# Kernel optimization log

Measured on AMD Instinct MI355X. Metric: run time of the kernel, lower is better.

Reference implementation:

```python
import jax, jax.numpy as jnp
import numpy as np

B, N, M, F = 32, 1024, 1024, 64


def setup_inputs() -> dict:
    key = jax.random.key(0)
    kx, ky = jax.random.split(key)
    x = jax.random.normal(kx, (B, N, F), dtype=jnp.float32)
    y = jax.random.normal(ky, (B, M, F), dtype=jnp.float32)
    return {"x": x, "y": y}


def _cdist(x, y):
    # torch.cdist(x, y, p=2): [N, M] euclidean distance matrix via GEMM form
    sq = (jnp.sum(x * x, axis=-1)[:, None]
          + jnp.sum(y * y, axis=-1)[None, :]
          - 2.0 * (x @ y.T))
    return jnp.sqrt(jnp.maximum(sq, 0.0))


def _dtw_single(x, y):
    # Classic DTW DP: D[i,j] = cost[i,j] + min(D[i-1,j], D[i,j-1], D[i-1,j-1])
    # with D[0,0]=0 and inf boundaries. The inner (j) recurrence
    #   cur[j] = cost[j] + min(m[j], cur[j-1]),  m[j] = min(prev[j], prev[j-1])
    # is a min-plus prefix scan solvable in closed form:
    #   cur[j] = C[j] + cummin_j(cost[j] + m[j] - C[j]),  C = cumsum(cost)
    # which vectorizes each row (wavefront-equivalent, no O(M) python loop).
    dist = _cdist(x, y)  # [N, M]
    m = dist.shape[1]
    init = jnp.concatenate([jnp.zeros((1,), dist.dtype),
                            jnp.full((m,), jnp.inf, dist.dtype)])  # D[0, :]

    def row_step(prev, cost_row):
        mins = jnp.minimum(prev[1:], prev[:-1])          # min(up, diag), [M]
        C = jnp.cumsum(cost_row)                         # [M]
        cur = C + jax.lax.cummin(cost_row + mins - C)    # [M]
        prev_new = jnp.concatenate(
            [jnp.full((1,), jnp.inf, dist.dtype), cur])  # D[i, 0] = inf
        return prev_new, None

    last, _ = jax.lax.scan(row_step, init, dist)
    return last[-1]  # D[N, M]


def reference(x, y):
    # batched forward, distances per pair: [B]
    return jax.vmap(_dtw_single)(x, y)
```

## Files before the change

### kernel.cpp

```cpp
#include <hip/hip_runtime.h>
#include <math.h>

#define BB 32
#define NN 1024
#define MM 1024
#define FF 64
#define INF_ 1e30f

typedef float f32x4 __attribute__((ext_vector_type(4)));

__global__ __launch_bounds__(256) void cost_kernel(const float* __restrict__ x,
                                                   const float* __restrict__ y,
                                                   float* __restrict__ cost) {
    __shared__ float Xs[FF][68];
    __shared__ float Ys[FF][68];
    __shared__ float xnl[64];
    __shared__ float ynl[64];
    const int b    = blockIdx.z;
    const int row0 = blockIdx.y * 64;
    const int col0 = blockIdx.x * 64;
    const int tid  = threadIdx.x;
    const float* xb = x + (size_t)b * NN * FF;
    const float* yb = y + (size_t)b * MM * FF;

    #pragma unroll
    for (int cc = 0; cc < 4; ++cc) {
        int s  = tid + cc * 256;
        int r  = s >> 4;
        int kq = s & 15;
        float4 vx = *(const float4*)(xb + (size_t)(row0 + r) * FF + kq * 4);
        float4 vy = *(const float4*)(yb + (size_t)(col0 + r) * FF + kq * 4);
        Xs[kq*4+0][r] = vx.x; Xs[kq*4+1][r] = vx.y; Xs[kq*4+2][r] = vx.z; Xs[kq*4+3][r] = vx.w;
        Ys[kq*4+0][r] = vy.x; Ys[kq*4+1][r] = vy.y; Ys[kq*4+2][r] = vy.z; Ys[kq*4+3][r] = vy.w;
    }
    __syncthreads();

    if (tid < 64) {
        float s = 0.0f;
        #pragma unroll 16
        for (int k = 0; k < FF; ++k) { float v = Xs[k][tid]; s += v * v; }
        xnl[tid] = s;
    } else if (tid < 128) {
        int r = tid - 64;
        float s = 0.0f;
        #pragma unroll 16
        for (int k = 0; k < FF; ++k) { float v = Ys[k][r]; s += v * v; }
        ynl[r] = s;
    }

    const int tx = tid & 15, ty = tid >> 4;
    float acc[4][4] = {};
    #pragma unroll 16
    for (int k = 0; k < FF; ++k) {
        float4 a  = *(const float4*)&Xs[k][ty * 4];
        float4 bb = *(const float4*)&Ys[k][tx * 4];
        float av[4] = {a.x, a.y, a.z, a.w};
        float bv[4] = {bb.x, bb.y, bb.z, bb.w};
        #pragma unroll
        for (int r = 0; r < 4; ++r)
            #pragma unroll
            for (int c = 0; c < 4; ++c)
                acc[r][c] += av[r] * bv[c];
    }
    __syncthreads();

    float* cD = cost + (size_t)b * NN * MM;
    #pragma unroll
    for (int r = 0; r < 4; ++r) {
        int rl  = ty * 4 + r;
        int row = row0 + rl;
        float xnv = xnl[rl];
        #pragma unroll
        for (int c = 0; c < 4; ++c) {
            int cl  = tx * 4 + c;
            int col = col0 + cl;
            float v = xnv + ynl[cl] - 2.0f * acc[r][c];
            v = sqrtf(fmaxf(v, 0.0f));
            cD[(size_t)((row + col) & 1023) * MM + row] = v;
        }
    }
}

__device__ __forceinline__ float dpp_wave_shr1(float v, float oldv) {
    int t = __builtin_amdgcn_update_dpp(__float_as_int(oldv), __float_as_int(v),
                                        0x138, 0xf, 0xf, false);
    return __int_as_float(t);
}

struct RowBuf { f32x4 q0, q1, q2, q3; };

__device__ __forceinline__ void issue_row(RowBuf& R, const float* rowbase,
                                          unsigned voff) {
    asm volatile(
        "global_load_dwordx4 %0, %4, %5\n\t"
        "global_load_dwordx4 %1, %4, %5 offset:16\n\t"
        "global_load_dwordx4 %2, %4, %5 offset:32\n\t"
        "global_load_dwordx4 %3, %4, %5 offset:48"
        : "=v"(R.q0), "=v"(R.q1), "=v"(R.q2), "=v"(R.q3)
        : "v"(voff), "s"(rowbase));
}

__device__ __forceinline__ void touch_row(float& dummy, const float* rowbase,
                                          unsigned voff) {
    asm volatile("global_load_dword %0, %1, %2"
                 : "+v"(dummy) : "v"(voff), "s"(rowbase));
}

__global__ __launch_bounds__(64)
__attribute__((amdgpu_waves_per_eu(1, 1)))
void dtw_diag_kernel(const float* __restrict__ cost, float* __restrict__ out) {
    const int b    = blockIdx.x;
    const int lane = threadIdx.x;
    const float* cbD = cost + (size_t)b * NN * MM;
    const unsigned voff = (unsigned)lane * 64u;

    RowBuf R0, R1, R2, R3, R4, R5, R6, R7;
    float dummy = 0.0f;
    issue_row(R0, cbD + 0 * (size_t)MM, voff);  touch_row(dummy, cbD +  8 * (size_t)MM, voff);
    issue_row(R1, cbD + 1 * (size_t)MM, voff);  touch_row(dummy, cbD +  9 * (size_t)MM, voff);
    issue_row(R2, cbD + 2 * (size_t)MM, voff);  touch_row(dummy, cbD + 10 * (size_t)MM, voff);
    issue_row(R3, cbD + 3 * (size_t)MM, voff);  touch_row(dummy, cbD + 11 * (size_t)MM, voff);
    issue_row(R4, cbD + 4 * (size_t)MM, voff);  touch_row(dummy, cbD + 12 * (size_t)MM, voff);
    issue_row(R5, cbD + 5 * (size_t)MM, voff);  touch_row(dummy, cbD + 13 * (size_t)MM, voff);
    issue_row(R6, cbD + 6 * (size_t)MM, voff);  touch_row(dummy, cbD + 14 * (size_t)MM, voff);
    issue_row(R7, cbD + 7 * (size_t)MM, voff);  touch_row(dummy, cbD + 15 * (size_t)MM, voff);

    float A[16], B[16];
    #pragma unroll
    for (int j = 0; j < 16; ++j) { A[j] = INF_; B[j] = INF_; }
    float bnd = 0.0f;

    #define DIAG_STEP(Rk, PV, P2, NR, NT)                                      \
    {                                                                          \
        float pvm1 = dpp_wave_shr1(PV[15], INF_);                              \
        float p2m1 = dpp_wave_shr1(P2[15], bnd);                               \
        float t[16];                                                           \
        _Pragma("unroll")                                                      \
        for (int r = 0; r < 16; ++r) {                                         \
            float pv_r = PV[r], p2_r = P2[r];                                  \
            t[r] = fminf(fminf(pv_r, pvm1), p2m1);                             \
            pvm1 = pv_r; p2m1 = p2_r;                                          \
        }                                                                      \
        asm volatile("s_waitcnt vmcnt(36)" ::: "memory");                      \
        __builtin_amdgcn_sched_barrier(0);                                     \
        float cc[16] = {Rk.q0[0], Rk.q0[1], Rk.q0[2], Rk.q0[3],                \
                        Rk.q1[0], Rk.q1[1], Rk.q1[2], Rk.q1[3],                \
                        Rk.q2[0], Rk.q2[1], Rk.q2[2], Rk.q2[3],                \
                        Rk.q3[0], Rk.q3[1], Rk.q3[2], Rk.q3[3]};               \
        _Pragma("unroll")                                                      \
        for (int r = 0; r < 16; ++r) P2[r] = cc[r] + t[r];                     \
        __builtin_amdgcn_sched_barrier(0);                                     \
        issue_row(Rk, cbD + (size_t)(NR) * MM, voff);                          \
        touch_row(dummy, cbD + (size_t)(NT) * MM, voff);                       \
    }

    DIAG_STEP(R0, A, B, 8,  16)   bnd = INF_;
    DIAG_STEP(R1, B, A, 9,  17)
    DIAG_STEP(R2, A, B, 10, 18)
    DIAG_STEP(R3, B, A, 11, 19)
    DIAG_STEP(R4, A, B, 12, 20)
    DIAG_STEP(R5, B, A, 13, 21)
    DIAG_STEP(R6, A, B, 14, 22)
    DIAG_STEP(R7, B, A, 15, 23)

    for (int d0 = 8; d0 < 2040; d0 += 8) {
        DIAG_STEP(R0, A, B, ((d0 +  8) & 1023), ((d0 + 16) & 1023))
        DIAG_STEP(R1, B, A, ((d0 +  9) & 1023), ((d0 + 17) & 1023))
        DIAG_STEP(R2, A, B, ((d0 + 10) & 1023), ((d0 + 18) & 1023))
        DIAG_STEP(R3, B, A, ((d0 + 11) & 1023), ((d0 + 19) & 1023))
        DIAG_STEP(R4, A, B, ((d0 + 12) & 1023), ((d0 + 20) & 1023))
        DIAG_STEP(R5, B, A, ((d0 + 13) & 1023), ((d0 + 21) & 1023))
        DIAG_STEP(R6, A, B, ((d0 + 14) & 1023), ((d0 + 22) & 1023))
        DIAG_STEP(R7, B, A, ((d0 + 15) & 1023), ((d0 + 23) & 1023))
    }

    DIAG_STEP(R0, A, B, 0, 16)
    DIAG_STEP(R1, B, A, 1, 17)
    DIAG_STEP(R2, A, B, 2, 18)
    DIAG_STEP(R3, B, A, 3, 19)
    DIAG_STEP(R4, A, B, 4, 20)
    DIAG_STEP(R5, B, A, 5, 21)
    DIAG_STEP(R6, A, B, 6, 22)
    #undef DIAG_STEP

    asm volatile("" :: "v"(dummy));

    if (lane == 63) out[b] = B[15];
}

__global__ __launch_bounds__(1024) void dtw_fused_kernel(const float* __restrict__ x,
                                                         const float* __restrict__ y,
                                                         float* __restrict__ out) {
    const int b    = blockIdx.x;
    const int tid  = threadIdx.x;
    const int lane = tid & 63;
    const int wid  = tid >> 6;
    __shared__ float P[MM];
    __shared__ float xrow[FF];
    __shared__ float part_sum[16];
    __shared__ float part_min[16];

    float yr[FF];
    const float* yrow = y + ((size_t)b * MM + tid) * FF;
    #pragma unroll
    for (int q = 0; q < FF / 4; ++q) {
        float4 v = ((const float4*)yrow)[q];
        yr[q*4+0] = v.x; yr[q*4+1] = v.y; yr[q*4+2] = v.z; yr[q*4+3] = v.w;
    }

    P[tid] = INF_;
    __syncthreads();

    const float* xb = x + (size_t)b * NN * FF;
    float result = 0.0f;

    for (int i = 0; i < NN; ++i) {
        if (tid < FF) xrow[tid] = xb[(size_t)i * FF + tid];
        float up   = P[tid];
        float diag = (tid == 0) ? (i == 0 ? 0.0f : INF_) : P[tid - 1];
        float m    = fminf(up, diag);
        __syncthreads();

        float ss = 0.0f;
        #pragma unroll 16
        for (int k = 0; k < FF; ++k) {
            float d = xrow[k] - yr[k];
            ss += d * d;
        }
        float c = sqrtf(ss);

        float s = c;
        #pragma unroll
        for (int d = 1; d < 64; d <<= 1) {
            float t = __shfl_up(s, d, 64);
            if (lane >= d) s += t;
        }
        if (lane == 63) part_sum[wid] = s;
        __syncthreads();
        if (tid < 16) {
            float p = part_sum[tid];
            #pragma unroll
            for (int d = 1; d < 16; d <<= 1) {
                float t = __shfl_up(p, d, 64);
                if (tid >= d) p += t;
            }
            part_sum[tid] = p;
        }
        __syncthreads();
        float C = s + (wid > 0 ? part_sum[wid - 1] : 0.0f);

        float z = c + m - C;
        float w = z;
        #pragma unroll
        for (int d = 1; d < 64; d <<= 1) {
            float t = __shfl_up(w, d, 64);
            if (lane >= d) w = fminf(w, t);
        }
        if (lane == 63) part_min[wid] = w;
        __syncthreads();
        if (tid < 16) {
            float p = part_min[tid];
            #pragma unroll
            for (int d = 1; d < 16; d <<= 1) {
                float t = __shfl_up(p, d, 64);
                if (tid >= d) p = fminf(p, t);
            }
            part_min[tid] = p;
        }
        __syncthreads();
        float wm  = (wid > 0) ? fminf(w, part_min[wid - 1]) : w;
        float cur = C + wm;

        P[tid] = cur;
        __syncthreads();
        if (i == NN - 1 && tid == MM - 1) result = cur;
    }
    if (tid == MM - 1) out[b] = result;
}

extern "C" void kernel_launch(void* const* d_in, const int* in_sizes, int n_in,
                              void* d_out, int out_size, void* d_ws, size_t ws_size,
                              hipStream_t stream) {
    const float* x = (const float*)d_in[0];
    const float* y = (const float*)d_in[1];
    float* out = (float*)d_out;

    size_t need = (size_t)BB * NN * MM * sizeof(float);

    if (ws_size >= need) {
        float* cost = (float*)d_ws;
        hipLaunchKernelGGL(cost_kernel, dim3(MM / 64, NN / 64, BB), dim3(256), 0, stream,
                           x, y, cost);
        hipLaunchKernelGGL(dtw_diag_kernel, dim3(BB), dim3(64), 0, stream, cost, out);
    } else {
        hipLaunchKernelGGL(dtw_fused_kernel, dim3(BB), dim3(1024), 0, stream, x, y, out);
    }
}
```

Measured before the change: 291.5 us.

## Store DTW cost matrix as bf16 and deepen diagonal prefetch pipeline

The cost kernel now writes the skewed cost matrix in bf16 (round-to-nearest-even), halving workspace traffic for both the write and the DTW scan's reads. The diagonal kernel loads half-size rows, unpacks them to fp32 in registers, and keeps 16 rows in flight instead of 8 plus touch prefetches, with the wait count adjusted to match. Accumulating 2047 bf16-rounded costs adds error to the final DTW distance, which may exceed tolerance.

```diff
diff --git a/kernel.cpp b/kernel.cpp
--- a/kernel.cpp
+++ b/kernel.cpp
@@ -11,7 +11,7 @@
 
 __global__ __launch_bounds__(256) void cost_kernel(const float* __restrict__ x,
                                                    const float* __restrict__ y,
-                                                   float* __restrict__ cost) {
+                                                   unsigned short* __restrict__ cost) {
     __shared__ float Xs[FF][68];
     __shared__ float Ys[FF][68];
     __shared__ float xnl[64];
@@ -64,7 +64,7 @@
     }
     __syncthreads();
 
-    float* cD = cost + (size_t)b * NN * MM;
+    unsigned short* cB = cost + (size_t)b * NN * MM;
     #pragma unroll
     for (int r = 0; r < 4; ++r) {
         int rl  = ty * 4 + r;
@@ -76,7 +76,9 @@
             int col = col0 + cl;
             float v = xnv + ynl[cl] - 2.0f * acc[r][c];
             v = sqrtf(fmaxf(v, 0.0f));
-            cD[(size_t)((row + col) & 1023) * MM + row] = v;
+            unsigned bb_ = __float_as_uint(v);
+            bb_ += 0x7FFFu + ((bb_ >> 16) & 1u);
+            cB[(size_t)((row + col) & 1023) * MM + row] = (unsigned short)(bb_ >> 16);
         }
     }
 }
@@ -87,50 +89,61 @@
     return __int_as_float(t);
 }
 
-struct RowBuf { f32x4 q0, q1, q2, q3; };
-
-__device__ __forceinline__ void issue_row(RowBuf& R, const float* rowbase,
-                                          unsigned voff) {
+struct RowBufB { f32x4 q0, q1; };
+
+__device__ __forceinline__ void issue_rowb(RowBufB& R, const unsigned short* rowbase,
+                                           unsigned voff) {
     asm volatile(
-        "global_load_dwordx4 %0, %4, %5\n\t"
-        "global_load_dwordx4 %1, %4, %5 offset:16\n\t"
-        "global_load_dwordx4 %2, %4, %5 offset:32\n\t"
-        "global_load_dwordx4 %3, %4, %5 offset:48"
-        : "=v"(R.q0), "=v"(R.q1), "=v"(R.q2), "=v"(R.q3)
+        "global_load_dwordx4 %0, %2, %3\n\t"
+        "global_load_dwordx4 %1, %2, %3 offset:16"
+        : "=v"(R.q0), "=v"(R.q1)
         : "v"(voff), "s"(rowbase));
 }
 
-__device__ __forceinline__ void touch_row(float& dummy, const float* rowbase,
-                                          unsigned voff) {
-    asm volatile("global_load_dword %0, %1, %2"
-                 : "+v"(dummy) : "v"(voff), "s"(rowbase));
+__device__ __forceinline__ void unpackb16(const RowBufB& R, float cc[16]) {
+    #pragma unroll
+    for (int q = 0; q < 4; ++q) {
+        unsigned w0 = __float_as_uint(R.q0[q]);
+        unsigned w1 = __float_as_uint(R.q1[q]);
+        cc[2*q+0]   = __uint_as_float(w0 << 16);
+        cc[2*q+1]   = __uint_as_float(w0 & 0xffff0000u);
+        cc[8+2*q+0] = __uint_as_float(w1 << 16);
+        cc[8+2*q+1] = __uint_as_float(w1 & 0xffff0000u);
+    }
 }
 
 __global__ __launch_bounds__(64)
 __attribute__((amdgpu_waves_per_eu(1, 1)))
-void dtw_diag_kernel(const float* __restrict__ cost, float* __restrict__ out) {
+void dtw_diag_kernel(const unsigned short* __restrict__ cost, float* __restrict__ out) {
     const int b    = blockIdx.x;
     const int lane = threadIdx.x;
-    const float* cbD = cost + (size_t)b * NN * MM;
-    const unsigned voff = (unsigned)lane * 64u;
-
-    RowBuf R0, R1, R2, R3, R4, R5, R6, R7;
-    float dummy = 0.0f;
-    issue_row(R0, cbD + 0 * (size_t)MM, voff);  touch_row(dummy, cbD +  8 * (size_t)MM, voff);
-    issue_row(R1, cbD + 1 * (size_t)MM, voff);  touch_row(dummy, cbD +  9 * (size_t)MM, voff);
-    issue_row(R2, cbD + 2 * (size_t)MM, voff);  touch_row(dummy, cbD + 10 * (size_t)MM, voff);
-    issue_row(R3, cbD + 3 * (size_t)MM, voff);  touch_row(dummy, cbD + 11 * (size_t)MM, voff);
-    issue_row(R4, cbD + 4 * (size_t)MM, voff);  touch_row(dummy, cbD + 12 * (size_t)MM, voff);
-    issue_row(R5, cbD + 5 * (size_t)MM, voff);  touch_row(dummy, cbD + 13 * (size_t)MM, voff);
-    issue_row(R6, cbD + 6 * (size_t)MM, voff);  touch_row(dummy, cbD + 14 * (size_t)MM, voff);
-    issue_row(R7, cbD + 7 * (size_t)MM, voff);  touch_row(dummy, cbD + 15 * (size_t)MM, voff);
+    const unsigned short* cbD = cost + (size_t)b * NN * MM;
+    const unsigned voff = (unsigned)lane * 32u;
+
+    RowBufB H0, H1, H2, H3, H4, H5, H6, H7, H8, H9, H10, H11, H12, H13, H14, H15;
+    issue_rowb(H0,  cbD +  0 * (size_t)MM, voff);
+    issue_rowb(H1,  cbD +  1 * (size_t)MM, voff);
+    issue_rowb(H2,  cbD +  2 * (size_t)MM, voff);
+    issue_rowb(H3,  cbD +  3 * (size_t)MM, voff);
+    issue_rowb(H4,  cbD +  4 * (size_t)MM, voff);
+    issue_rowb(H5,  cbD +  5 * (size_t)MM, voff);
+    issue_rowb(H6,  cbD +  6 * (size_t)MM, voff);
+    issue_rowb(H7,  cbD +  7 * (size_t)MM, voff);
+    issue_rowb(H8,  cbD +  8 * (size_t)MM, voff);
+    issue_rowb(H9,  cbD +  9 * (size_t)MM, voff);
+    issue_rowb(H10, cbD + 10 * (size_t)MM, voff);
+    issue_rowb(H11, cbD + 11 * (size_t)MM, voff);
+    issue_rowb(H12, cbD + 12 * (size_t)MM, voff);
+    issue_rowb(H13, cbD + 13 * (size_t)MM, voff);
+    issue_rowb(H14, cbD + 14 * (size_t)MM, voff);
+    issue_rowb(H15, cbD + 15 * (size_t)MM, voff);
 
     float A[16], B[16];
     #pragma unroll
     for (int j = 0; j < 16; ++j) { A[j] = INF_; B[j] = INF_; }
     float bnd = 0.0f;
 
-    #define DIAG_STEP(Rk, PV, P2, NR, NT)                                      \
+    #define DIAG_STEP(Hk, PV, P2, NR)                                          \
     {                                                                          \
         float pvm1 = dpp_wave_shr1(PV[15], INF_);                              \
         float p2m1 = dpp_wave_shr1(P2[15], bnd);                               \
@@ -141,49 +154,67 @@
             t[r] = fminf(fminf(pv_r, pvm1), p2m1);                             \
             pvm1 = pv_r; p2m1 = p2_r;                                          \
         }                                                                      \
-        asm volatile("s_waitcnt vmcnt(36)" ::: "memory");                      \
+        asm volatile("s_waitcnt vmcnt(30)" ::: "memory");                      \
         __builtin_amdgcn_sched_barrier(0);                                     \
-        float cc[16] = {Rk.q0[0], Rk.q0[1], Rk.q0[2], Rk.q0[3],                \
-                        Rk.q1[0], Rk.q1[1], Rk.q1[2], Rk.q1[3],                \
-                        Rk.q2[0], Rk.q2[1], Rk.q2[2], Rk.q2[3],                \
-                        Rk.q3[0], Rk.q3[1], Rk.q3[2], Rk.q3[3]};               \
+        float cc[16]; unpackb16(Hk, cc);                                       \
         _Pragma("unroll")                                                      \
         for (int r = 0; r < 16; ++r) P2[r] = cc[r] + t[r];                     \
         __builtin_amdgcn_sched_barrier(0);                                     \
-        issue_row(Rk, cbD + (size_t)(NR) * MM, voff);                          \
-        touch_row(dummy, cbD + (size_t)(NT) * MM, voff);                       \
-    }
-
-    DIAG_STEP(R0, A, B, 8,  16)   bnd = INF_;
-    DIAG_STEP(R1, B, A, 9,  17)
-    DIAG_STEP(R2, A, B, 10, 18)
-    DIAG_STEP(R3, B, A, 11, 19)
-    DIAG_STEP(R4, A, B, 12, 20)
-    DIAG_STEP(R5, B, A, 13, 21)
-    DIAG_STEP(R6, A, B, 14, 22)
-    DIAG_STEP(R7, B, A, 15, 23)
-
-    for (int d0 = 8; d0 < 2040; d0 += 8) {
-        DIAG_STEP(R0, A, B, ((d0 +  8) & 1023), ((d0 + 16) & 1023))
-        DIAG_STEP(R1, B, A, ((d0 +  9) & 1023), ((d0 + 17) & 1023))
-        DIAG_STEP(R2, A, B, ((d0 + 10) & 1023), ((d0 + 18) & 1023))
-        DIAG_STEP(R3, B, A, ((d0 + 11) & 1023), ((d0 + 19) & 1023))
-        DIAG_STEP(R4, A, B, ((d0 + 12) & 1023), ((d0 + 20) & 1023))
-        DIAG_STEP(R5, B, A, ((d0 + 13) & 1023), ((d0 + 21) & 1023))
-        DIAG_STEP(R6, A, B, ((d0 + 14) & 1023), ((d0 + 22) & 1023))
-        DIAG_STEP(R7, B, A, ((d0 + 15) & 1023), ((d0 + 23) & 1023))
-    }
-
-    DIAG_STEP(R0, A, B, 0, 16)
-    DIAG_STEP(R1, B, A, 1, 17)
-    DIAG_STEP(R2, A, B, 2, 18)
-    DIAG_STEP(R3, B, A, 3, 19)
-    DIAG_STEP(R4, A, B, 4, 20)
-    DIAG_STEP(R5, B, A, 5, 21)
-    DIAG_STEP(R6, A, B, 6, 22)
+        issue_rowb(Hk, cbD + (size_t)(NR) * MM, voff);                         \
+    }
+
+    DIAG_STEP(H0,  A, B, 16)   bnd = INF_;
+    DIAG_STEP(H1,  B, A, 17)
+    DIAG_STEP(H2,  A, B, 18)
+    DIAG_STEP(H3,  B, A, 19)
+    DIAG_STEP(H4,  A, B, 20)
+    DIAG_STEP(H5,  B, A, 21)
+    DIAG_STEP(H6,  A, B, 22)
+    DIAG_STEP(H7,  B, A, 23)
+    DIAG_STEP(H8,  A, B, 24)
+    DIAG_STEP(H9,  B, A, 25)
+    DIAG_STEP(H10, A, B, 26)
+    DIAG_STEP(H11, B, A, 27)
+    DIAG_STEP(H12, A, B, 28)
+    DIAG_STEP(H13, B, A, 29)
+    DIAG_STEP(H14, A, B, 30)
+    DIAG_STEP(H15, B, A, 31)
+
+    for (int d0 = 16; d0 < 2032; d0 += 16) {
+        DIAG_STEP(H0,  A, B, ((d0 + 16) & 1023))
+        DIAG_STEP(H1,  B, A, ((d0 + 17) & 1023))
+        DIAG_STEP(H2,  A, B, ((d0 + 18) & 1023))
+        DIAG_STEP(H3,  B, A, ((d0 + 19) & 1023))
+        DIAG_STEP(H4,  A, B, ((d0 + 20) & 1023))
+        DIAG_STEP(H5,  B, A, ((d0 + 21) & 1023))
+        DIAG_STEP(H6,  A, B, ((d0 + 22) & 1023))
+        DIAG_STEP(H7,  B, A, ((d0 + 23) & 1023))
+        DIAG_STEP(H8,  A, B, ((d0 + 24) & 1023))
+        DIAG_STEP(H9,  B, A, ((d0 + 25) & 1023))
+        DIAG_STEP(H10, A, B, ((d0 + 26) & 1023))
+        DIAG_STEP(H11, B, A, ((d0 + 27) & 1023))
+        DIAG_STEP(H12, A, B, ((d0 + 28) & 1023))
+        DIAG_STEP(H13, B, A, ((d0 + 29) & 1023))
+        DIAG_STEP(H14, A, B, ((d0 + 30) & 1023))
+        DIAG_STEP(H15, B, A, ((d0 + 31) & 1023))
+    }
+
+    DIAG_STEP(H0,  A, B, 0)
+    DIAG_STEP(H1,  B, A, 1)
+    DIAG_STEP(H2,  A, B, 2)
+    DIAG_STEP(H3,  B, A, 3)
+    DIAG_STEP(H4,  A, B, 4)
+    DIAG_STEP(H5,  B, A, 5)
+    DIAG_STEP(H6,  A, B, 6)
+    DIAG_STEP(H7,  B, A, 7)
+    DIAG_STEP(H8,  A, B, 8)
+    DIAG_STEP(H9,  B, A, 9)
+    DIAG_STEP(H10, A, B, 10)
+    DIAG_STEP(H11, B, A, 11)
+    DIAG_STEP(H12, A, B, 12)
+    DIAG_STEP(H13, B, A, 13)
+    DIAG_STEP(H14, A, B, 14)
     #undef DIAG_STEP
-
-    asm volatile("" :: "v"(dummy));
 
     if (lane == 63) out[b] = B[15];
 }
@@ -285,10 +316,10 @@
     const float* y = (const float*)d_in[1];
     float* out = (float*)d_out;
 
-    size_t need = (size_t)BB * NN * MM * sizeof(float);
+    size_t need = (size_t)BB * NN * MM * sizeof(unsigned short);
 
     if (ws_size >= need) {
-        float* cost = (float*)d_ws;
+        unsigned short* cost = (unsigned short*)d_ws;
         hipLaunchKernelGGL(cost_kernel, dim3(MM / 64, NN / 64, BB), dim3(256), 0, stream,
                            x, y, cost);
         hipLaunchKernelGGL(dtw_diag_kernel, dim3(BB), dim3(64), 0, stream, cost, out);
```

Result: slower. 318.0 us (+9.1%).
